# Kernel tuning notes

Hardware: AMD Instinct MI355X
Metric: run time of the kernel (lower is better)

Reference implementation:

```python
import jax, jax.numpy as jnp
import numpy as np
from jax import lax

B, CIN, H, W = 8, 256, 64, 64
CC = 128          # corr_channels
COUT = 64         # out_channels
KH = KW = 5       # corr_kernel_size
SH = SW = 1       # corr_stride
PT, PB = KH // 2, (KH + 1) // 2 - 1   # pad='k'
PL, PR = KW // 2, (KW + 1) // 2 - 1


def setup_inputs() -> dict:
    key = jax.random.key(0)
    k1, k2, k3, k4, k5 = jax.random.split(key, 5)
    x = jax.random.normal(k1, (B, CIN, H, W), dtype=jnp.float32)
    w_ext = jax.random.normal(k2, (CC, CIN, 3, 3), dtype=jnp.float32) * 0.02
    b_ext = jax.random.normal(k3, (CC,), dtype=jnp.float32) * 0.02
    w_reg = jax.random.normal(k4, (COUT, CC, KH, KW), dtype=jnp.float32) * 0.02
    b_reg = jax.random.normal(k5, (COUT,), dtype=jnp.float32) * 0.02
    return {"x": x, "w_ext": w_ext, "b_ext": b_ext, "w_reg": w_reg, "b_reg": b_reg}


def _forward(x, w_ext, b_ext, w_reg, b_reg):
    # feature extraction: 3x3 conv, padding 1
    f = lax.conv_general_dilated(x, w_ext, (1, 1), ((1, 1), (1, 1)))
    f = f + b_ext[None, :, None, None]
    # local autocorrelation: multiply each window element by the window center, per channel
    fp = jnp.pad(f, ((0, 0), (0, 0), (PT, PB), (PL, PR)))
    nH = (fp.shape[2] - KH) // SH + 1
    nW = (fp.shape[3] - KW) // SW + 1
    center = fp[:, :, KH // 2:KH // 2 + nH * SH:SH, KW // 2:KW // 2 + nW * SW:SW]  # [B,CC,nH,nW]
    patches = jnp.stack(
        [fp[:, :, u:u + nH * SH:SH, v:v + nW * SW:SW] for u in range(KH) for v in range(KW)],
        axis=-1)  # [B,CC,nH,nW,KH*KW]
    corr = patches * center[..., None]  # [B,CC,nH,nW,KH*KW]
    out = jnp.einsum('bcijk,ock->bijo', corr, w_reg.reshape(COUT, CC, KH * KW))
    out = out + b_reg
    return out.transpose(0, 3, 1, 2)  # permute=True -> [B, COUT, nH, nW]


def reference(x, w_ext, b_ext, w_reg, b_reg):
    return _forward(x, w_ext, b_ext, w_reg, b_reg)
```

## Files before the change

### kernel.cpp

```cpp
#include <hip/hip_runtime.h>
#include <hip/hip_bf16.h>

#define B_    8
#define CIN_  256
#define CC_   128
#define COUT_ 64
#define HP_   68
#define HPX_  (HP_ * HP_)
#define XQW_  66
#define XQPX_ (XQW_ * XQW_)

typedef __attribute__((ext_vector_type(8))) short bh8;
typedef __attribute__((ext_vector_type(4))) float f4;

__device__ __forceinline__ ushort f2bf(float f) {
    uint u = __float_as_uint(f);
    return (ushort)((u + 0x7fffu + ((u >> 16) & 1u)) >> 16);
}
__device__ __forceinline__ float bf2f(ushort s) {
    return __uint_as_float(((uint)s) << 16);
}
__device__ __forceinline__ short f2bf_c(float f) {
    __hip_bfloat16 h = __float2bfloat16(f);
    short s;
    __builtin_memcpy(&s, &h, 2);
    return s;
}

#define NB_MISC 2217
__global__ __launch_bounds__(256) void prep_all(const float* __restrict__ x,
                                                const float* __restrict__ w_ext,
                                                const float* __restrict__ w_reg,
                                                short* __restrict__ wg,
                                                short* __restrict__ wa,
                                                ushort* __restrict__ fpad_t,
                                                ushort* __restrict__ xq) {
    __shared__ float xt[2][32][65];
    const int tid = threadIdx.x;
    if (blockIdx.x < NB_MISC) {
        int e = blockIdx.x * 256 + tid;
        if (e < 67584) {
            int seg = e & 15;
            int t = e >> 4;
            int b = t / 528, rp = t - b * 528;
            int i, j;
            if (rp < 136) { i = rp / 68; j = rp - (rp / 68) * 68; }
            else if (rp < 272) { int r = rp - 136; i = 66 + r / 68; j = r - (r / 68) * 68; }
            else { int r = rp - 272; i = 2 + (r >> 2); int c = r & 3; j = (c < 2) ? c : c + 64; }
            uint4 z; z.x = 0u; z.y = 0u; z.z = 0u; z.w = 0u;
            *(uint4*)&fpad_t[(((size_t)b * HPX_) + i * HP_ + j) * 128 + seg * 8] = z;
            return;
        }
        e -= 67584;
        if (e < 294912) {
            int ci = e & 31;
            int t  = e >> 5;
            int cc = t & 127;
            int t2 = t >> 7;
            int rs = t2 % 9, cb = t2 / 9;
            wg[e] = (short)f2bf(w_ext[(cc * CIN_ + cb * 32 + ci) * 9 + rs]);
            return;
        }
        e -= 294912;
        if (e < 204800) {
            int ci = e & 31;
            int o  = (e >> 5) & 63;
            int rest = e >> 11;
            int k = rest % 25, q = rest / 25;
            wa[e] = (short)f2bf(w_reg[(o * CC_ + q * 32 + ci) * 25 + k]);
        }
        return;
    }

    const int pid = blockIdx.x - NB_MISC;
    const int rp = pid % 33, cb = (pid / 33) & 7, b = pid / 264;

#pragma unroll
    for (int rr = 0; rr < 2; ++rr) {
        int y = rp * 2 + rr - 1;
        if ((unsigned)y < 64u) {
            int xx = tid & 63, wv = tid >> 6;
#pragma unroll
            for (int it = 0; it < 8; ++it) {
                int ci = it * 4 + wv;
                xt[rr][ci][xx] = x[(((size_t)(b * CIN_ + cb * 32 + ci)) * 64 + y) * 64 + xx];
            }
        }
    }
    __syncthreads();

    for (int e = tid; e < 528; e += 256) {
        int rr = e / 264, t = e - rr * 264;
        int hc = t >> 2, seg = t & 3;
        int y = rp * 2 + rr - 1, xx = hc - 1;
        uint pk[4] = {0u, 0u, 0u, 0u};
        if ((unsigned)y < 64u && (unsigned)xx < 64u) {
#pragma unroll
            for (int i = 0; i < 4; ++i) {
                uint lo = f2bf(xt[rr][seg * 8 + i * 2][xx]);
                uint hi = f2bf(xt[rr][seg * 8 + i * 2 + 1][xx]);
                pk[i] = lo | (hi << 16);
            }
        }
        uint4 v; v.x = pk[0]; v.y = pk[1]; v.z = pk[2]; v.w = pk[3];
        *(uint4*)&xq[((((size_t)(b * 8 + cb)) * XQPX_) + (rp * 2 + rr) * XQW_ + hc) * 32 + seg * 8] = v;
    }
}

__global__ __launch_bounds__(256)
__attribute__((amdgpu_waves_per_eu(2, 2)))
void conv3x3_mfma(const ushort* __restrict__ xq,
                  const short* __restrict__ wg,
                  const float* __restrict__ bext,
                  ushort* __restrict__ fpad_t) {
    __shared__ __align__(16) short xh[2][100 * 72];
    __shared__ __align__(16) short wlds[2][3 * 128 * 32];
    const int tid = threadIdx.x;
    const int lane = tid & 63, wv = tid >> 6;
    const int j0 = blockIdx.x * 8, i0 = blockIdx.y * 8, b = blockIdx.z;
    const int l15 = lane & 15, kg = lane >> 4;
    const int cc0 = wv * 32;

    int abase[2];
#pragma unroll
    for (int mm = 0; mm < 2; ++mm) {
        int cc = cc0 + mm * 16 + l15;
        abase[mm] = cc * 32 + ((((cc >> 1) + kg) & 3) << 3);
    }
    int xb[4];
#pragma unroll
    for (int nn = 0; nn < 4; ++nn) {
        int px = nn * 16 + l15, pi = px >> 3, pj = px & 7;
        xb[nn] = (pi * 10 + pj) * 72 + kg * 8;
    }
    int wdst[6]; int goff[6];
#pragma unroll
    for (int k = 0; k < 6; ++k) {
        int c = tid + k * 256;
        int cc = (c & 511) >> 2, kgc = c & 3;
        wdst[k] = (c >> 9) * 4096 + cc * 32 + ((((cc >> 1) + kgc) & 3) << 3);
        goff[k] = c * 8;
    }
    const int hp0 = tid >> 2, seg0 = tid & 3;
    const int hr0 = hp0 / 10, hc0 = hp0 - hr0 * 10;
    const int xsrc0 = ((i0 + hr0) * XQW_ + (j0 + hc0)) * 32 + seg0 * 8;
    const int xdst0 = hp0 * 72 + seg0 * 8;
    const int hp1 = (tid + 256) >> 2;
    const int hr1 = hp1 / 10, hc1 = hp1 - hr1 * 10;
    const int xsrc1 = ((i0 + hr1) * XQW_ + (j0 + hc1)) * 32 + seg0 * 8;
    const int xdst1 = hp1 * 72 + seg0 * 8;
    const bool x1ok = tid < 144;

    f4 acc[2][4] = {};

    {
#pragma unroll
        for (int k = 0; k < 6; ++k)
            *(bh8*)&wlds[0][wdst[k]] = *(const bh8*)(wg + goff[k]);
        const ushort* xbase = xq + (((size_t)(b * 8 + 0)) * XQPX_) * 32;
        *(bh8*)&xh[0][xdst0] = *(const bh8*)&xbase[xsrc0];
        if (x1ok) *(bh8*)&xh[0][xdst1] = *(const bh8*)&xbase[xsrc1];
    }
    __syncthreads();

    int p = 0;
#pragma unroll 1
    for (int cb = 0; cb < 8; ++cb) {
        const int xbuf = cb & 1;
#pragma unroll 1
        for (int g = 0; g < 3; ++g) {
            const int buf = p & 1;
            const bool wmore = (p < 23);
            const bool xmore = (g == 2) && (cb < 7);

            bh8 wreg[6];
            const short* gsrc = wg + (size_t)(wmore ? (p + 1) : 23) * 12288;
#pragma unroll
            for (int k = 0; k < 6; ++k)
                wreg[k] = *(const bh8*)(gsrc + goff[k]);
            bh8 xr0, xr1;
            if (xmore) {
                const ushort* xbase = xq + (((size_t)(b * 8 + cb + 1)) * XQPX_) * 32;
                xr0 = *(const bh8*)&xbase[xsrc0];
                if (x1ok) xr1 = *(const bh8*)&xbase[xsrc1];
            }

            const short* wb = wlds[buf];
            const int goffs = g * 10 * 72;
#pragma unroll
            for (int s = 0; s < 3; ++s) {
                bh8 a[2], bb[4];
#pragma unroll
                for (int mm = 0; mm < 2; ++mm)
                    a[mm] = *(const bh8*)&wb[s * 4096 + abase[mm]];
#pragma unroll
                for (int nn = 0; nn < 4; ++nn)
                    bb[nn] = *(const bh8*)&xh[xbuf][xb[nn] + goffs + s * 72];
#pragma unroll
                for (int mm = 0; mm < 2; ++mm)
#pragma unroll
                    for (int nn = 0; nn < 4; ++nn)
                        acc[mm][nn] = __builtin_amdgcn_mfma_f32_16x16x32_bf16(
                            a[mm], bb[nn], acc[mm][nn], 0, 0, 0);
            }

            if (wmore) {
#pragma unroll
                for (int k = 0; k < 6; ++k)
                    *(bh8*)&wlds[buf ^ 1][wdst[k]] = wreg[k];
            }
            if (xmore) {
                *(bh8*)&xh[xbuf ^ 1][xdst0] = xr0;
                if (x1ok) *(bh8*)&xh[xbuf ^ 1][xdst1] = xr1;
            }
            __syncthreads();
            ++p;
        }
    }

#pragma unroll
    for (int mm = 0; mm < 2; ++mm) {
        const int ccb = cc0 + mm * 16 + kg * 4;
        float bv0 = bext[ccb + 0], bv1 = bext[ccb + 1];
        float bv2 = bext[ccb + 2], bv3 = bext[ccb + 3];
#pragma unroll
        for (int nn = 0; nn < 4; ++nn) {
            int px = nn * 16 + l15, pi = px >> 3, pj = px & 7;
            size_t row = (size_t)b * HPX_ + (2 + i0 + pi) * HP_ + (2 + j0 + pj);
            uint lo = (uint)f2bf(acc[mm][nn][0] + bv0) | ((uint)f2bf(acc[mm][nn][1] + bv1) << 16);
            uint hi = (uint)f2bf(acc[mm][nn][2] + bv2) | ((uint)f2bf(acc[mm][nn][3] + bv3) << 16);
            uint2 pk; pk.x = lo; pk.y = hi;
            *(uint2*)&fpad_t[row * 128 + ccb] = pk;
        }
    }
}

__global__ __launch_bounds__(256)
__attribute__((amdgpu_waves_per_eu(2, 2)))
void autocorr_mfma(const ushort* __restrict__ ft,
                   const short* __restrict__ wA,
                   const float* __restrict__ breg,
                   float* __restrict__ out) {
    __shared__ __align__(16) short flds[144 * 136];
    __shared__ __align__(16) short wlds[2][5 * 64 * 32];
    const int tid = threadIdx.x;
    const int lane = tid & 63, wv = tid >> 6;
    const int oh = wv >> 1, ph = wv & 1;
    const int j0 = blockIdx.x * 8, i0 = blockIdx.y * 8, b = blockIdx.z;
    const int l15 = lane & 15, kg = lane >> 4;

    int abase[2];
#pragma unroll
    for (int mm = 0; mm < 2; ++mm) {
        int o = oh * 32 + mm * 16 + l15;
        abase[mm] = o * 32 + ((((o >> 1) + kg) & 3) << 3);
    }
    int wdst[5]; int goff[5];
#pragma unroll
    for (int k = 0; k < 5; ++k) {
        int c = tid + k * 256;
        int o = (c & 255) >> 2, kgc = c & 3;
        wdst[k] = (c >> 8) * 2048 + o * 32 + ((((o >> 1) + kgc) & 3) << 3);
        goff[k] = c * 8;
    }

    for (int e = tid; e < 2304; e += 256) {
        int hp = e >> 4, seg = e & 15;
        int hr = hp / 12, hc = hp - hr * 12;
        const ushort* src = ft + ((size_t)b * HPX_ + (i0 + hr) * HP_ + (j0 + hc)) * 128 + seg * 8;
        *(bh8*)&flds[hp * 136 + seg * 8] = *(const bh8*)src;
    }
#pragma unroll
    for (int k = 0; k < 5; ++k)
        *(bh8*)&wlds[0][wdst[k]] = *(const bh8*)(wA + goff[k]);
    __syncthreads();

    f4 acc[2][2] = {};
    int base_off[2], cen_off[2];
#pragma unroll
    for (int t = 0; t < 2; ++t) {
        int px = ph * 32 + t * 16 + l15;
        int pi = px >> 3, pj = px & 7;
        base_off[t] = (pi * 12 + pj) * 136 + kg * 8;
        cen_off[t]  = ((pi + 2) * 12 + (pj + 2)) * 136 + kg * 8;
    }

    int p = 0;
#pragma unroll 1
    for (int q = 0; q < 4; ++q) {
        float cen[2][8];
#pragma unroll
        for (int t = 0; t < 2; ++t) {
            bh8 c8 = *(const bh8*)&flds[cen_off[t] + q * 32];
#pragma unroll
            for (int jj = 0; jj < 8; ++jj) cen[t][jj] = bf2f((ushort)c8[jj]);
        }
#pragma unroll 1
        for (int u = 0; u < 5; ++u) {
            const int buf = p & 1;
            const bool wmore = (p < 19);

            bh8 wreg[5];
            const short* gsrc = wA + (size_t)(wmore ? (p + 1) : 19) * 10240;
#pragma unroll
            for (int k = 0; k < 5; ++k)
                wreg[k] = *(const bh8*)(gsrc + goff[k]);

            const short* wb = wlds[buf];
#pragma unroll
            for (int v = 0; v < 5; ++v) {
                const int koff = (u * 12 + v) * 136;
                bh8 a[2];
#pragma unroll
                for (int mm = 0; mm < 2; ++mm)
                    a[mm] = *(const bh8*)&wb[v * 2048 + abase[mm]];
                bh8 bb[2];
#pragma unroll
                for (int t = 0; t < 2; ++t) {
                    bh8 s8 = *(const bh8*)&flds[base_off[t] + q * 32 + koff];
#pragma unroll
                    for (int jj = 0; jj < 8; ++jj) {
                        float pr = bf2f((ushort)s8[jj]) * cen[t][jj];
                        bb[t][jj] = f2bf_c(pr);
                    }
                }
#pragma unroll
                for (int mm = 0; mm < 2; ++mm)
#pragma unroll
                    for (int t = 0; t < 2; ++t)
                        acc[mm][t] = __builtin_amdgcn_mfma_f32_16x16x32_bf16(
                            a[mm], bb[t], acc[mm][t], 0, 0, 0);
            }

            if (wmore) {
#pragma unroll
                for (int k = 0; k < 5; ++k)
                    *(bh8*)&wlds[buf ^ 1][wdst[k]] = wreg[k];
            }
            __syncthreads();
            ++p;
        }
    }

#pragma unroll
    for (int mm = 0; mm < 2; ++mm) {
#pragma unroll
        for (int reg = 0; reg < 4; ++reg) {
            int o = oh * 32 + mm * 16 + kg * 4 + reg;
            float bv = breg[o];
#pragma unroll
            for (int t = 0; t < 2; ++t) {
                int px = ph * 32 + t * 16 + l15, pi = px >> 3, pj = px & 7;
                out[(((size_t)(b * COUT_ + o)) * 64 + i0 + pi) * 64 + j0 + pj] =
                    acc[mm][t][reg] + bv;
            }
        }
    }
}

extern "C" void kernel_launch(void* const* d_in, const int* in_sizes, int n_in,
                              void* d_out, int out_size, void* d_ws, size_t ws_size,
                              hipStream_t stream) {
    const float* x     = (const float*)d_in[0];
    const float* w_ext = (const float*)d_in[1];
    const float* b_ext = (const float*)d_in[2];
    const float* w_reg = (const float*)d_in[3];
    const float* b_reg = (const float*)d_in[4];
    float* out = (float*)d_out;

    char* ws = (char*)d_ws;
    const size_t FPADT_BYTES = (size_t)B_ * HPX_ * 128 * 2;
    const size_t WG_BYTES    = (size_t)8 * 9 * 128 * 32 * 2;
    const size_t WA_BYTES    = (size_t)4 * 25 * 64 * 32 * 2;
    ushort* fpad_t = (ushort*)ws;
    short*  wgq    = (short*)(ws + FPADT_BYTES);
    short*  wa     = (short*)(ws + FPADT_BYTES + WG_BYTES);
    ushort* xq     = (ushort*)(ws + FPADT_BYTES + WG_BYTES + WA_BYTES);

    prep_all<<<NB_MISC + 33 * 8 * 8, 256, 0, stream>>>(x, w_ext, w_reg, wgq, wa, fpad_t, xq);

    dim3 grid(8, 8, 8);
    conv3x3_mfma<<<grid, 256, 0, stream>>>(xq, wgq, b_ext, fpad_t);
    autocorr_mfma<<<grid, 256, 0, stream>>>(fpad_t, wa, b_reg, out);
}
```

Before: 77.41 us.

## Widen autocorr tile to 8x16 pixels with 512-thread blocks

The autocorrelation kernel now gives each block an 8x16 pixel tile instead of 8x8 and runs 8 waves (512 threads) instead of 4. The block shares one weight double-buffer across twice as many pixels, so weight traffic from global memory to LDS per output pixel is halved and the halo overhead per pixel shrinks. In exchange the grid halves to 256 blocks, leaving fewer blocks to spread across CUs. LDS use per block also grows, and the waves_per_eu hint combined with the larger block may change occupancy.

```diff
diff --git a/kernel.cpp b/kernel.cpp
--- a/kernel.cpp
+++ b/kernel.cpp
@@ -235,18 +235,18 @@
     }
 }
 
-__global__ __launch_bounds__(256)
+__global__ __launch_bounds__(512)
 __attribute__((amdgpu_waves_per_eu(2, 2)))
 void autocorr_mfma(const ushort* __restrict__ ft,
                    const short* __restrict__ wA,
                    const float* __restrict__ breg,
                    float* __restrict__ out) {
-    __shared__ __align__(16) short flds[144 * 136];
+    __shared__ __align__(16) short flds[240 * 136];
     __shared__ __align__(16) short wlds[2][5 * 64 * 32];
     const int tid = threadIdx.x;
     const int lane = tid & 63, wv = tid >> 6;
-    const int oh = wv >> 1, ph = wv & 1;
-    const int j0 = blockIdx.x * 8, i0 = blockIdx.y * 8, b = blockIdx.z;
+    const int oh = wv >> 2, pxg = wv & 3;
+    const int j0 = blockIdx.x * 16, i0 = blockIdx.y * 8, b = blockIdx.z;
     const int l15 = lane & 15, kg = lane >> 4;
 
     int abase[2];
@@ -255,34 +255,35 @@
         int o = oh * 32 + mm * 16 + l15;
         abase[mm] = o * 32 + ((((o >> 1) + kg) & 3) << 3);
     }
-    int wdst[5]; int goff[5];
-#pragma unroll
-    for (int k = 0; k < 5; ++k) {
-        int c = tid + k * 256;
+    int wdst[3]; int goff[3];
+#pragma unroll
+    for (int k = 0; k < 3; ++k) {
+        int c = tid + k * 512;
         int o = (c & 255) >> 2, kgc = c & 3;
         wdst[k] = (c >> 8) * 2048 + o * 32 + ((((o >> 1) + kgc) & 3) << 3);
         goff[k] = c * 8;
     }
-
-    for (int e = tid; e < 2304; e += 256) {
+    const bool w3 = tid < 256;
+
+    for (int e = tid; e < 3840; e += 512) {
         int hp = e >> 4, seg = e & 15;
-        int hr = hp / 12, hc = hp - hr * 12;
+        int hr = hp / 20, hc = hp - hr * 20;
         const ushort* src = ft + ((size_t)b * HPX_ + (i0 + hr) * HP_ + (j0 + hc)) * 128 + seg * 8;
         *(bh8*)&flds[hp * 136 + seg * 8] = *(const bh8*)src;
     }
-#pragma unroll
-    for (int k = 0; k < 5; ++k)
-        *(bh8*)&wlds[0][wdst[k]] = *(const bh8*)(wA + goff[k]);
+    *(bh8*)&wlds[0][wdst[0]] = *(const bh8*)(wA + goff[0]);
+    *(bh8*)&wlds[0][wdst[1]] = *(const bh8*)(wA + goff[1]);
+    if (w3) *(bh8*)&wlds[0][wdst[2]] = *(const bh8*)(wA + goff[2]);
     __syncthreads();
 
     f4 acc[2][2] = {};
     int base_off[2], cen_off[2];
 #pragma unroll
     for (int t = 0; t < 2; ++t) {
-        int px = ph * 32 + t * 16 + l15;
-        int pi = px >> 3, pj = px & 7;
-        base_off[t] = (pi * 12 + pj) * 136 + kg * 8;
-        cen_off[t]  = ((pi + 2) * 12 + (pj + 2)) * 136 + kg * 8;
+        int px = pxg * 32 + t * 16 + l15;
+        int pi = px >> 4, pj = px & 15;
+        base_off[t] = (pi * 20 + pj) * 136 + kg * 8;
+        cen_off[t]  = ((pi + 2) * 20 + (pj + 2)) * 136 + kg * 8;
     }
 
     int p = 0;
@@ -300,16 +301,16 @@
             const int buf = p & 1;
             const bool wmore = (p < 19);
 
-            bh8 wreg[5];
+            bh8 wreg0, wreg1, wreg2;
             const short* gsrc = wA + (size_t)(wmore ? (p + 1) : 19) * 10240;
-#pragma unroll
-            for (int k = 0; k < 5; ++k)
-                wreg[k] = *(const bh8*)(gsrc + goff[k]);
+            wreg0 = *(const bh8*)(gsrc + goff[0]);
+            wreg1 = *(const bh8*)(gsrc + goff[1]);
+            if (w3) wreg2 = *(const bh8*)(gsrc + goff[2]);
 
             const short* wb = wlds[buf];
 #pragma unroll
             for (int v = 0; v < 5; ++v) {
-                const int koff = (u * 12 + v) * 136;
+                const int koff = (u * 20 + v) * 136;
                 bh8 a[2];
 #pragma unroll
                 for (int mm = 0; mm < 2; ++mm)
@@ -333,9 +334,9 @@
             }
 
             if (wmore) {
-#pragma unroll
-                for (int k = 0; k < 5; ++k)
-                    *(bh8*)&wlds[buf ^ 1][wdst[k]] = wreg[k];
+                *(bh8*)&wlds[buf ^ 1][wdst[0]] = wreg0;
+                *(bh8*)&wlds[buf ^ 1][wdst[1]] = wreg1;
+                if (w3) *(bh8*)&wlds[buf ^ 1][wdst[2]] = wreg2;
             }
             __syncthreads();
             ++p;
@@ -350,7 +351,7 @@
             float bv = breg[o];
 #pragma unroll
             for (int t = 0; t < 2; ++t) {
-                int px = ph * 32 + t * 16 + l15, pi = px >> 3, pj = px & 7;
+                int px = pxg * 32 + t * 16 + l15, pi = px >> 4, pj = px & 15;
                 out[(((size_t)(b * COUT_ + o)) * 64 + i0 + pi) * 64 + j0 + pj] =
                     acc[mm][t][reg] + bv;
             }
@@ -379,7 +380,8 @@
 
     prep_all<<<NB_MISC + 33 * 8 * 8, 256, 0, stream>>>(x, w_ext, w_reg, wgq, wa, fpad_t, xq);
 
-    dim3 grid(8, 8, 8);
-    conv3x3_mfma<<<grid, 256, 0, stream>>>(xq, wgq, b_ext, fpad_t);
-    autocorr_mfma<<<grid, 256, 0, stream>>>(fpad_t, wa, b_reg, out);
-}
+    dim3 cgrid(8, 8, 8);
+    conv3x3_mfma<<<cgrid, 256, 0, stream>>>(xq, wgq, b_ext, fpad_t);
+    dim3 agrid(4, 8, 8);
+    autocorr_mfma<<<agrid, 512, 0, stream>>>(fpad_t, wa, b_reg, out);
+}
```

After: 74.29 us, median of 2. -4.0%, faster.

## Split autocorr over channel halves with wider 8x16 tiles and atomic accumulation

Applied to the files above, without the earlier changes.

The autocorrelation kernel now uses 8x16 pixel tiles and splits the 128 correlation channels into two halves across blocks (grid z doubled). Each wave computes all 64 output channels for 32 pixels, so the halo overhead per pixel falls and each weight load from LDS feeds more MFMAs. The two partial sums are combined with relaxed float atomics into an output that prep_all now zero-fills. This adds an output-clearing pass and atomic traffic, and the summation order is no longer fixed.

```diff
diff --git a/kernel.cpp b/kernel.cpp
--- a/kernel.cpp
+++ b/kernel.cpp
@@ -27,14 +27,15 @@
     return s;
 }
 
-#define NB_MISC 2217
+#define NB_MISC 4264
 __global__ __launch_bounds__(256) void prep_all(const float* __restrict__ x,
                                                 const float* __restrict__ w_ext,
                                                 const float* __restrict__ w_reg,
                                                 short* __restrict__ wg,
                                                 short* __restrict__ wa,
                                                 ushort* __restrict__ fpad_t,
-                                                ushort* __restrict__ xq) {
+                                                ushort* __restrict__ xq,
+                                                float* __restrict__ out) {
     __shared__ float xt[2][32][65];
     const int tid = threadIdx.x;
     if (blockIdx.x < NB_MISC) {
@@ -68,6 +69,12 @@
             int rest = e >> 11;
             int k = rest % 25, q = rest / 25;
             wa[e] = (short)f2bf(w_reg[(o * CC_ + q * 32 + ci) * 25 + k]);
+            return;
+        }
+        e -= 204800;
+        if (e < 524288) {
+            float4 z; z.x = 0.f; z.y = 0.f; z.z = 0.f; z.w = 0.f;
+            *(float4*)&out[(size_t)e * 4] = z;
         }
         return;
     }
@@ -241,18 +248,18 @@
                    const short* __restrict__ wA,
                    const float* __restrict__ breg,
                    float* __restrict__ out) {
-    __shared__ __align__(16) short flds[144 * 136];
+    __shared__ __align__(16) short flds[240 * 72];
     __shared__ __align__(16) short wlds[2][5 * 64 * 32];
     const int tid = threadIdx.x;
     const int lane = tid & 63, wv = tid >> 6;
-    const int oh = wv >> 1, ph = wv & 1;
-    const int j0 = blockIdx.x * 8, i0 = blockIdx.y * 8, b = blockIdx.z;
+    const int j0 = blockIdx.x * 16, i0 = blockIdx.y * 8;
+    const int b = blockIdx.z >> 1, h = blockIdx.z & 1;
     const int l15 = lane & 15, kg = lane >> 4;
 
-    int abase[2];
-#pragma unroll
-    for (int mm = 0; mm < 2; ++mm) {
-        int o = oh * 32 + mm * 16 + l15;
+    int abase[4];
+#pragma unroll
+    for (int mm = 0; mm < 4; ++mm) {
+        int o = mm * 16 + l15;
         abase[mm] = o * 32 + ((((o >> 1) + kg) & 3) << 3);
     }
     int wdst[5]; int goff[5];
@@ -263,45 +270,46 @@
         wdst[k] = (c >> 8) * 2048 + o * 32 + ((((o >> 1) + kgc) & 3) << 3);
         goff[k] = c * 8;
     }
-
-    for (int e = tid; e < 2304; e += 256) {
-        int hp = e >> 4, seg = e & 15;
-        int hr = hp / 12, hc = hp - hr * 12;
-        const ushort* src = ft + ((size_t)b * HPX_ + (i0 + hr) * HP_ + (j0 + hc)) * 128 + seg * 8;
-        *(bh8*)&flds[hp * 136 + seg * 8] = *(const bh8*)src;
+    const short* wbase_g = wA + (size_t)h * 102400;
+
+    for (int e = tid; e < 1920; e += 256) {
+        int hp = e >> 3, seg = e & 7;
+        int hr = hp / 20, hc = hp - hr * 20;
+        const ushort* src = ft + ((size_t)b * HPX_ + (i0 + hr) * HP_ + (j0 + hc)) * 128 + (h * 8 + seg) * 8;
+        *(bh8*)&flds[hp * 72 + seg * 8] = *(const bh8*)src;
     }
 #pragma unroll
     for (int k = 0; k < 5; ++k)
-        *(bh8*)&wlds[0][wdst[k]] = *(const bh8*)(wA + goff[k]);
+        *(bh8*)&wlds[0][wdst[k]] = *(const bh8*)(wbase_g + goff[k]);
     __syncthreads();
 
-    f4 acc[2][2] = {};
+    f4 acc[4][2] = {};
     int base_off[2], cen_off[2];
 #pragma unroll
     for (int t = 0; t < 2; ++t) {
-        int px = ph * 32 + t * 16 + l15;
-        int pi = px >> 3, pj = px & 7;
-        base_off[t] = (pi * 12 + pj) * 136 + kg * 8;
-        cen_off[t]  = ((pi + 2) * 12 + (pj + 2)) * 136 + kg * 8;
+        int px = wv * 32 + t * 16 + l15;
+        int pi = px >> 4, pj = px & 15;
+        base_off[t] = (pi * 20 + pj) * 72 + kg * 8;
+        cen_off[t]  = ((pi + 2) * 20 + (pj + 2)) * 72 + kg * 8;
     }
 
     int p = 0;
 #pragma unroll 1
-    for (int q = 0; q < 4; ++q) {
+    for (int qq = 0; qq < 2; ++qq) {
         float cen[2][8];
 #pragma unroll
         for (int t = 0; t < 2; ++t) {
-            bh8 c8 = *(const bh8*)&flds[cen_off[t] + q * 32];
+            bh8 c8 = *(const bh8*)&flds[cen_off[t] + qq * 32];
 #pragma unroll
             for (int jj = 0; jj < 8; ++jj) cen[t][jj] = bf2f((ushort)c8[jj]);
         }
 #pragma unroll 1
         for (int u = 0; u < 5; ++u) {
             const int buf = p & 1;
-            const bool wmore = (p < 19);
+            const bool wmore = (p < 9);
 
             bh8 wreg[5];
-            const short* gsrc = wA + (size_t)(wmore ? (p + 1) : 19) * 10240;
+            const short* gsrc = wbase_g + (size_t)(wmore ? (p + 1) : 9) * 10240;
 #pragma unroll
             for (int k = 0; k < 5; ++k)
                 wreg[k] = *(const bh8*)(gsrc + goff[k]);
@@ -309,15 +317,15 @@
             const short* wb = wlds[buf];
 #pragma unroll
             for (int v = 0; v < 5; ++v) {
-                const int koff = (u * 12 + v) * 136;
-                bh8 a[2];
-#pragma unroll
-                for (int mm = 0; mm < 2; ++mm)
+                const int koff = (u * 20 + v) * 72;
+                bh8 a[4];
+#pragma unroll
+                for (int mm = 0; mm < 4; ++mm)
                     a[mm] = *(const bh8*)&wb[v * 2048 + abase[mm]];
                 bh8 bb[2];
 #pragma unroll
                 for (int t = 0; t < 2; ++t) {
-                    bh8 s8 = *(const bh8*)&flds[base_off[t] + q * 32 + koff];
+                    bh8 s8 = *(const bh8*)&flds[base_off[t] + qq * 32 + koff];
 #pragma unroll
                     for (int jj = 0; jj < 8; ++jj) {
                         float pr = bf2f((ushort)s8[jj]) * cen[t][jj];
@@ -325,7 +333,7 @@
                     }
                 }
 #pragma unroll
-                for (int mm = 0; mm < 2; ++mm)
+                for (int mm = 0; mm < 4; ++mm)
 #pragma unroll
                     for (int t = 0; t < 2; ++t)
                         acc[mm][t] = __builtin_amdgcn_mfma_f32_16x16x32_bf16(
@@ -343,16 +351,17 @@
     }
 
 #pragma unroll
-    for (int mm = 0; mm < 2; ++mm) {
+    for (int mm = 0; mm < 4; ++mm) {
 #pragma unroll
         for (int reg = 0; reg < 4; ++reg) {
-            int o = oh * 32 + mm * 16 + kg * 4 + reg;
-            float bv = breg[o];
+            int o = mm * 16 + kg * 4 + reg;
+            float bv = (h == 0) ? breg[o] : 0.f;
 #pragma unroll
             for (int t = 0; t < 2; ++t) {
-                int px = ph * 32 + t * 16 + l15, pi = px >> 3, pj = px & 7;
-                out[(((size_t)(b * COUT_ + o)) * 64 + i0 + pi) * 64 + j0 + pj] =
-                    acc[mm][t][reg] + bv;
+                int px = wv * 32 + t * 16 + l15, pi = px >> 4, pj = px & 15;
+                float* dst = &out[(((size_t)(b * COUT_ + o)) * 64 + i0 + pi) * 64 + j0 + pj];
+                __hip_atomic_fetch_add(dst, acc[mm][t][reg] + bv,
+                                       __ATOMIC_RELAXED, __HIP_MEMORY_SCOPE_AGENT);
             }
         }
     }
@@ -377,9 +386,10 @@
     short*  wa     = (short*)(ws + FPADT_BYTES + WG_BYTES);
     ushort* xq     = (ushort*)(ws + FPADT_BYTES + WG_BYTES + WA_BYTES);
 
-    prep_all<<<NB_MISC + 33 * 8 * 8, 256, 0, stream>>>(x, w_ext, w_reg, wgq, wa, fpad_t, xq);
-
-    dim3 grid(8, 8, 8);
-    conv3x3_mfma<<<grid, 256, 0, stream>>>(xq, wgq, b_ext, fpad_t);
-    autocorr_mfma<<<grid, 256, 0, stream>>>(fpad_t, wa, b_reg, out);
-}
+    prep_all<<<NB_MISC + 33 * 8 * 8, 256, 0, stream>>>(x, w_ext, w_reg, wgq, wa, fpad_t, xq, out);
+
+    dim3 cgrid(8, 8, 8);
+    conv3x3_mfma<<<cgrid, 256, 0, stream>>>(xq, wgq, b_ext, fpad_t);
+    dim3 agrid(4, 8, 16);
+    autocorr_mfma<<<agrid, 256, 0, stream>>>(fpad_t, wa, b_reg, out);
+}
```

Measured after the change: 80.09 us. 3.5% more time.
